# Optimization experiments

Hardware: AMD Instinct MI355X
Metric: run time of the kernel (lower is better)

Reference implementation:

```python
import jax, jax.numpy as jnp
import numpy as np
import math

NUM_HEADS = 16
NUM_KV_HEADS = 4
HEAD_DIM = 128
ROPE_THETA = 10000.0


def rotate_half(x):
    half = x.shape[-1] // 2
    return jnp.concatenate((-x[..., half:], x[..., :half]), axis=-1)


def setup_inputs() -> dict:
    key = jax.random.key(0)
    ks = jax.random.split(key, 5)
    B, S, H = 2, 2048, 2048
    hidden_states = jax.random.normal(ks[0], (B, S, H), dtype=jnp.float32)
    scale = 1.0 / math.sqrt(H)
    wq = jax.random.normal(ks[1], (NUM_HEADS * HEAD_DIM, H), dtype=jnp.float32) * scale
    wk = jax.random.normal(ks[2], (NUM_KV_HEADS * HEAD_DIM, H), dtype=jnp.float32) * scale
    wv = jax.random.normal(ks[3], (NUM_KV_HEADS * HEAD_DIM, H), dtype=jnp.float32) * scale
    wo = jax.random.normal(ks[4], (H, NUM_HEADS * HEAD_DIM), dtype=jnp.float32) * scale
    # additive causal mask [B,1,S,S]
    causal = jnp.where(jnp.tril(jnp.ones((S, S), dtype=bool)), 0.0, -1e9).astype(jnp.float32)
    attention_mask = jnp.broadcast_to(causal[None, None], (B, 1, S, S))
    position_ids = jnp.broadcast_to(jnp.arange(S, dtype=jnp.int64)[None], (B, S))
    return {
        'hidden_states': hidden_states, 'wq': wq, 'wk': wk, 'wv': wv, 'wo': wo,
        'attention_mask': attention_mask, 'position_ids': position_ids,
    }


def reference(hidden_states, wq, wk, wv, wo, attention_mask, position_ids):
    B, S, H = hidden_states.shape
    nh, nkv, hd = NUM_HEADS, NUM_KV_HEADS, HEAD_DIM
    groups = nh // nkv

    # projections (torch Linear: x @ W^T)
    q = (hidden_states @ wq.T).reshape(B, S, nh, hd).transpose(0, 2, 1, 3)   # [B,nh,S,hd]
    k = (hidden_states @ wk.T).reshape(B, S, nkv, hd).transpose(0, 2, 1, 3)  # [B,nkv,S,hd]
    v = (hidden_states @ wv.T).reshape(B, S, nkv, hd).transpose(0, 2, 1, 3)

    # RoPE: cos/sin gathered by position_ids -> [B,1,S,hd]
    inv_freq = 1.0 / (ROPE_THETA ** (jnp.arange(0, hd, 2, dtype=jnp.float32) / hd))  # [hd/2]
    freqs = position_ids.astype(jnp.float32)[:, :, None] * inv_freq                  # [B,S,hd/2]
    emb = jnp.concatenate((freqs, freqs), axis=-1)                                   # [B,S,hd]
    cos = jnp.cos(emb)[:, None]
    sin = jnp.sin(emb)[:, None]
    q = q * cos + rotate_half(q) * sin
    k = k * cos + rotate_half(k) * sin

    # GQA: repeat kv heads
    k = jnp.repeat(k, groups, axis=1)  # [B,nh,S,hd]
    v = jnp.repeat(v, groups, axis=1)

    scores = jnp.einsum('bhqd,bhkd->bhqk', q, k) / math.sqrt(hd) + attention_mask
    attn = jax.nn.softmax(scores.astype(jnp.float32), axis=-1).astype(q.dtype)
    ctx = jnp.einsum('bhqk,bhkd->bhqd', attn, v)            # [B,nh,S,hd]
    ctx = ctx.transpose(0, 2, 1, 3).reshape(B, S, nh * hd)  # [B,S,H]
    out = ctx @ wo.T
    return out
```

## Files before the change

### kernel.cpp

```cpp
#include <hip/hip_runtime.h>
#include <hip/hip_bf16.h>
#include <stdint.h>

typedef __bf16 bf16x8 __attribute__((ext_vector_type(8)));
typedef float f32x4 __attribute__((ext_vector_type(4)));
typedef float f32x16 __attribute__((ext_vector_type(16)));

#define NH 16
#define NKV 4
#define HD 128
#define HQ (NH*HD)
#define HKV (NKV*HD)
#define LDX 3072

__device__ __forceinline__ void gl_lds16(const void* g, void* l) {
  __builtin_amdgcn_global_load_lds(
      (const __attribute__((address_space(1))) void*)g,
      (__attribute__((address_space(3))) void*)l, 16, 0, 0);
}

__device__ __forceinline__ uint32_t pk2(float lo, float hi) {
  union { __hip_bfloat16 h[2]; uint32_t u; } x;
  x.h[0] = __float2bfloat16(lo);
  x.h[1] = __float2bfloat16(hi);
  return x.u;
}

__global__ void k_cast_all(const float* __restrict__ hs, const float* __restrict__ wq,
                           const float* __restrict__ wk, const float* __restrict__ wv,
                           const float* __restrict__ wo,
                           __hip_bfloat16* __restrict__ Xb, __hip_bfloat16* __restrict__ Wqb,
                           __hip_bfloat16* __restrict__ Wkb, __hip_bfloat16* __restrict__ Wvb,
                           __hip_bfloat16* __restrict__ Wob) {
  int i = blockIdx.x * blockDim.x + threadIdx.x;
  const float* src; __hip_bfloat16* dst; int off;
  if (i < 2097152)      { src = hs; dst = Xb;  off = i; }
  else if (i < 3145728) { src = wq; dst = Wqb; off = i - 2097152; }
  else if (i < 3407872) { src = wk; dst = Wkb; off = i - 3145728; }
  else if (i < 3670016) { src = wv; dst = Wvb; off = i - 3407872; }
  else                  { src = wo; dst = Wob; off = i - 3670016; }
  float4 v = reinterpret_cast<const float4*>(src)[off];
  union { __hip_bfloat16 b[4]; ushort4 u; } o;
  o.b[0] = __float2bfloat16(v.x); o.b[1] = __float2bfloat16(v.y);
  o.b[2] = __float2bfloat16(v.z); o.b[3] = __float2bfloat16(v.w);
  reinterpret_cast<ushort4*>(dst)[off] = o.u;
}

__global__ void k_rope_vt(__hip_bfloat16* __restrict__ X, __hip_bfloat16* __restrict__ Vt,
                          const int* __restrict__ pid, int S) {
  __shared__ __hip_bfloat16 tile[32][33];
  const int RB = 4096;
  if (blockIdx.x < RB) {
    int idx = blockIdx.x * 256 + threadIdx.x;
    int i = idx & 63;
    int hh = (idx >> 6) & 3;
    int tok = idx >> 8;
    bool is64 = (pid[1] == 0);
    int pos = is64 ? pid[2 * tok] : pid[tok];
    float f = (float)pos * __expf(-(float)i * (9.210340371976184f / 64.0f));
    float sn, cs;
    __sincosf(f, &sn, &cs);
    size_t base = (size_t)tok * LDX + 2048 + hh * 128;
    float x0 = __bfloat162float(X[base + i]);
    float x1 = __bfloat162float(X[base + 64 + i]);
    X[base + i]      = __float2bfloat16(x0 * cs - x1 * sn);
    X[base + 64 + i] = __float2bfloat16(x1 * cs + x0 * sn);
  } else {
    int bb = blockIdx.x - RB;
    int bkv = bb >> 8;
    int rem = bb & 255;
    int s0 = (rem & 63) * 32, d0 = (rem >> 6) * 32;
    int b = bkv >> 2, kvh = bkv & 3;
    int tx = threadIdx.x & 31, ty = threadIdx.x >> 5;
    for (int i = 0; i < 32; i += 8)
      tile[ty + i][tx] = X[((size_t)(b * S) + s0 + ty + i) * LDX + 2560 + kvh * 128 + d0 + tx];
    __syncthreads();
    for (int i = 0; i < 32; i += 8)
      Vt[((size_t)bkv * 128 + d0 + ty + i) * S + s0 + tx] = tile[tx][ty + i];
  }
}

__global__ __launch_bounds__(512, 1) void k_gemmQKV(
    const __hip_bfloat16* __restrict__ A, const __hip_bfloat16* __restrict__ B,
    __hip_bfloat16* __restrict__ C, int Nld, int K) {
  __shared__ __hip_bfloat16 As[2][2][256 * 32];
  __shared__ __hip_bfloat16 Bs[2][2][192 * 32];

  const int t = threadIdx.x, w = t >> 6, l = t & 63;
  const int lr = l & 15, lg = l >> 4;
  const int wr = w >> 2, wc = w & 3;

  const int bid = blockIdx.x;
  const int id2 = (bid & 7) * 32 + (bid >> 3);
  const int bm = id2 & 15, bn = id2 >> 4;

  const __hip_bfloat16* Ap = A + (size_t)(bm * 256) * K;
  const __hip_bfloat16* Bp = B + (size_t)(bn * 192) * K;

  auto stageA = [&](__hip_bfloat16* lp, int kt, int kk) {
#pragma unroll
    for (int inst = 0; inst < 2; ++inst) {
      const int chunk = inst * 512 + t;
      const int row = chunk >> 2, c_st = chunk & 3;
      const int c_nat = c_st ^ ((row >> 1) & 3);
      gl_lds16(Ap + (size_t)row * K + kt * 64 + kk * 32 + c_nat * 8,
               lp + (size_t)(inst * 512 + (w << 6)) * 8);
    }
  };
  auto stageB = [&](__hip_bfloat16* lp, int kt, int kk) {
    {
      const int chunk = t;
      const int row = chunk >> 2, c_st = chunk & 3;
      const int c_nat = c_st ^ ((row >> 1) & 3);
      gl_lds16(Bp + (size_t)row * K + kt * 64 + kk * 32 + c_nat * 8,
               lp + (size_t)(w << 6) * 8);
    }
    if (w < 4) {
      const int chunk = 512 + t;
      const int row = chunk >> 2, c_st = chunk & 3;
      const int c_nat = c_st ^ ((row >> 1) & 3);
      gl_lds16(Bp + (size_t)row * K + kt * 64 + kk * 32 + c_nat * 8,
               lp + (size_t)(512 + (w << 6)) * 8);
    }
  };
  auto waitTile = [&](int wv) {
    if (wv < 4) asm volatile("s_waitcnt vmcnt(4)" ::: "memory");
    else        asm volatile("s_waitcnt vmcnt(3)" ::: "memory");
  };

  f32x4 acc[8][3] = {};
  const int nt = K >> 6;

  stageA(As[0][0], 0, 0);
  stageB(Bs[0][0], 0, 0);
  stageA(As[0][1], 0, 1);
  stageB(Bs[0][1], 0, 1);
  stageA(As[1][0], 1, 0);
  stageB(Bs[1][0], 1, 0);
  waitTile(w);
  __builtin_amdgcn_s_barrier();
  asm volatile("" ::: "memory");

  for (int tt = 0; tt < nt; ++tt) {
    const int cur = tt & 1;
    const int nx1 = (tt + 1 < nt) ? tt + 1 : nt - 1;
    const int nx2 = (tt + 2 < nt) ? tt + 2 : nt - 1;
#pragma unroll
    for (int kk = 0; kk < 2; ++kk) {
      bf16x8 aF[8], bF[3];
#pragma unroll
      for (int n = 0; n < 3; ++n) {
        int rB = wc * 48 + n * 16 + lr;
        bF[n] = *reinterpret_cast<const bf16x8*>(
            &Bs[cur][kk][rB * 32 + (lg ^ ((rB >> 1) & 3)) * 8]);
      }
#pragma unroll
      for (int m8 = 0; m8 < 8; ++m8) {
        int rA = wr * 128 + (m8 >> 2) * 64 + (m8 & 3) * 16 + lr;
        aF[m8] = *reinterpret_cast<const bf16x8*>(
            &As[cur][kk][rA * 32 + (lg ^ ((rA >> 1) & 3)) * 8]);
      }
      if (kk == 0) { stageA(As[nx1 & 1][1], nx1, 1); stageB(Bs[nx1 & 1][1], nx1, 1); }
      else         { stageA(As[nx2 & 1][0], nx2, 0); stageB(Bs[nx2 & 1][0], nx2, 0); }
      asm volatile("" ::: "memory");
      __builtin_amdgcn_s_barrier();
      asm volatile("" ::: "memory");
      __builtin_amdgcn_s_setprio(1);
#pragma unroll
      for (int m8 = 0; m8 < 8; ++m8)
#pragma unroll
        for (int n = 0; n < 3; ++n)
          acc[m8][n] = __builtin_amdgcn_mfma_f32_16x16x32_bf16(
              aF[m8], bF[n], acc[m8][n], 0, 0, 0);
      __builtin_amdgcn_s_setprio(0);
      if (kk == 1) waitTile(w);
      asm volatile("" ::: "memory");
      __builtin_amdgcn_s_barrier();
      asm volatile("" ::: "memory");
    }
  }

  const int row0 = bm * 256 + wr * 128;
  const int col0 = bn * 192 + wc * 48;
#pragma unroll
  for (int m = 0; m < 8; ++m)
#pragma unroll
    for (int n = 0; n < 3; ++n)
#pragma unroll
      for (int r = 0; r < 4; ++r)
        C[(size_t)(row0 + (m >> 2) * 64 + (m & 3) * 16 + lg * 4 + r) * Nld +
          col0 + n * 16 + lr] = __float2bfloat16(acc[m][n][r]);
}

__global__ __launch_bounds__(512, 1) void k_gemmO(
    const __hip_bfloat16* __restrict__ A, const __hip_bfloat16* __restrict__ B,
    float* __restrict__ C, int N, int K) {
  __shared__ __hip_bfloat16 As[2][2][128 * 32];
  __shared__ __hip_bfloat16 Bs[2][2][256 * 32];

  const int t = threadIdx.x, w = t >> 6, l = t & 63;
  const int lr = l & 15, lg = l >> 4;
  const int wr = w >> 2, wc = w & 3;

  const int bid = blockIdx.x;
  const int id2 = (bid & 7) * 32 + (bid >> 3);
  const int bm = id2 & 31, bn = id2 >> 5;

  const __hip_bfloat16* Ap = A + (size_t)(bm * 128) * K;
  const __hip_bfloat16* Bp = B + (size_t)(bn * 256) * K;

  auto stageA = [&](__hip_bfloat16* lp, int kt, int kk) {
    const int row = t >> 2, c_st = t & 3;
    const int c_nat = c_st ^ ((row >> 1) & 3);
    gl_lds16(Ap + (size_t)row * K + kt * 64 + kk * 32 + c_nat * 8,
             lp + (size_t)(w << 6) * 8);
  };
  auto stageB = [&](__hip_bfloat16* lp, int kt, int kk) {
#pragma unroll
    for (int inst = 0; inst < 2; ++inst) {
      const int chunk = inst * 512 + t;
      const int row = chunk >> 2, c_st = chunk & 3;
      const int c_nat = c_st ^ ((row >> 1) & 3);
      gl_lds16(Bp + (size_t)row * K + kt * 64 + kk * 32 + c_nat * 8,
               lp + (size_t)(inst * 512 + (w << 6)) * 8);
    }
  };

  f32x4 acc[4][4] = {};
  const int nt = K >> 6;

  stageA(As[0][0], 0, 0);
  stageB(Bs[0][0], 0, 0);
  stageA(As[0][1], 0, 1);
  stageB(Bs[0][1], 0, 1);
  stageA(As[1][0], 1, 0);
  stageB(Bs[1][0], 1, 0);
  asm volatile("s_waitcnt vmcnt(3)" ::: "memory");
  __builtin_amdgcn_s_barrier();
  asm volatile("" ::: "memory");

  for (int tt = 0; tt < nt; ++tt) {
    const int cur = tt & 1;
    const int nx1 = (tt + 1 < nt) ? tt + 1 : nt - 1;
    const int nx2 = (tt + 2 < nt) ? tt + 2 : nt - 1;
#pragma unroll
    for (int kk = 0; kk < 2; ++kk) {
      bf16x8 aF[4], bF[4];
#pragma unroll
      for (int n = 0; n < 4; ++n) {
        int rB = wc * 64 + n * 16 + lr;
        bF[n] = *reinterpret_cast<const bf16x8*>(
            &Bs[cur][kk][rB * 32 + (lg ^ ((rB >> 1) & 3)) * 8]);
      }
#pragma unroll
      for (int m4 = 0; m4 < 4; ++m4) {
        int rA = wr * 64 + (m4 >> 1) * 32 + (m4 & 1) * 16 + lr;
        aF[m4] = *reinterpret_cast<const bf16x8*>(
            &As[cur][kk][rA * 32 + (lg ^ ((rA >> 1) & 3)) * 8]);
      }
      if (kk == 0) { stageA(As[nx1 & 1][1], nx1, 1); stageB(Bs[nx1 & 1][1], nx1, 1); }
      else         { stageA(As[nx2 & 1][0], nx2, 0); stageB(Bs[nx2 & 1][0], nx2, 0); }
      asm volatile("" ::: "memory");
      __builtin_amdgcn_s_barrier();
      asm volatile("" ::: "memory");
      __builtin_amdgcn_s_setprio(1);
#pragma unroll
      for (int m4 = 0; m4 < 4; ++m4)
#pragma unroll
        for (int n = 0; n < 4; ++n)
          acc[m4][n] = __builtin_amdgcn_mfma_f32_16x16x32_bf16(
              aF[m4], bF[n], acc[m4][n], 0, 0, 0);
      __builtin_amdgcn_s_setprio(0);
      if (kk == 1) asm volatile("s_waitcnt vmcnt(3)" ::: "memory");
      asm volatile("" ::: "memory");
      __builtin_amdgcn_s_barrier();
      asm volatile("" ::: "memory");
    }
  }

  const int row0 = bm * 128 + wr * 64;
  const int col0 = bn * 256 + wc * 64;
#pragma unroll
  for (int m = 0; m < 4; ++m)
#pragma unroll
    for (int n = 0; n < 4; ++n)
#pragma unroll
      for (int r = 0; r < 4; ++r)
        C[(size_t)(row0 + m * 16 + lg * 4 + r) * N + col0 + n * 16 + lr] =
            acc[m][n][r];
}

__global__ __launch_bounds__(256, 2) void k_attn(
    const __hip_bfloat16* __restrict__ X, const __hip_bfloat16* __restrict__ Vt,
    const int* __restrict__ pid, __hip_bfloat16* __restrict__ ctx, int S) {
  __shared__ __hip_bfloat16 SM[32768];

  const int bid = blockIdx.x;
  const int g  = bid & 7;
  const int idx = bid >> 3;
  int hi, jj;
  if (idx < 32) { hi = idx >> 4;              jj = idx & 15; }
  else          { hi = 2 + ((idx - 32) >> 4); jj = 15 - ((idx - 32) & 15); }
  const int b = g >> 2, kvh = g & 3;
  const int h = kvh * 4 + hi;

  const int t = threadIdx.x, w = t >> 6, l = t & 63;
  const int q = l & 31, hf = l >> 5;
  const int qt64 = (w < 2) ? jj : (31 - jj);
  const int q0w = qt64 * 64 + (w & 1) * 32;
  const int nt = 32 - jj;
  const float c1 = 0.12752511f;
  const float M0 = 48.0f;

  const __hip_bfloat16* Qp = X + ((size_t)(b * S) + q0w + q) * LDX + h * 128 + hf * 8;
  bf16x8 aq[8];
#pragma unroll
  for (int mq = 0; mq < 8; ++mq)
    aq[mq] = *reinterpret_cast<const bf16x8*>(Qp + mq * 16);

  {
    bool is64 = (pid[1] == 0);
    int toki = b * S + q0w + q;
    int pos = is64 ? pid[2 * toki] : pid[toki];
    float fpos = (float)pos;
#pragma unroll
    for (int mq = 0; mq < 4; ++mq)
#pragma unroll
      for (int j = 0; j < 8; ++j) {
        int fi = mq * 16 + hf * 8 + j;
        float ang = fpos * __expf((float)fi * (-9.210340371976184f / 64.0f));
        float sn, cs;
        __sincosf(ang, &sn, &cs);
        float x0 = (float)aq[mq][j];
        float x1 = (float)aq[mq + 4][j];
        aq[mq][j]     = (__bf16)(x0 * cs - x1 * sn);
        aq[mq + 4][j] = (__bf16)(x1 * cs + x0 * sn);
      }
  }

  const __hip_bfloat16* KG = X + (size_t)(b * S) * LDX + 2048 + kvh * 128;
  const __hip_bfloat16* VG = Vt + ((size_t)(b * NKV + kvh) * 128) * S;

  auto stageK = [&](int buf, int kv0) {
#pragma unroll
    for (int j = 0; j < 4; ++j) {
      int off16 = (w * 4 + j) * 64 + l;
      int row = off16 >> 4;
      int c_nat = (off16 & 15) ^ ((row >> 1) & 15);
      gl_lds16(KG + (size_t)(kv0 + row) * LDX + c_nat * 8,
               &SM[buf * 8192 + (w * 4 + j) * 512]);
    }
  };
  auto stageV = [&](int buf, int kv0) {
#pragma unroll
    for (int j = 0; j < 4; ++j) {
      int off16 = (w * 4 + j) * 64 + l;
      int d = off16 >> 3;
      int c_nat = (off16 & 7) ^ ((d >> 2) & 7);
      gl_lds16(VG + (size_t)d * S + kv0 + c_nat * 8,
               &SM[16384 + buf * 8192 + (w * 4 + j) * 512]);
    }
  };

  f32x16 O[4] = {};
  float l_i = 0.0f;

  stageK(0, 0); stageV(0, 0);
  int cur = 0;
  for (int tkv = 0; tkv < nt; ++tkv) {
    const int kv0 = tkv * 64;
    if (tkv + 1 < nt) {
      stageK(cur ^ 1, kv0 + 64);
      stageV(cur ^ 1, kv0 + 64);
      asm volatile("s_waitcnt vmcnt(8)" ::: "memory");
    } else {
      asm volatile("s_waitcnt vmcnt(0)" ::: "memory");
    }
    __builtin_amdgcn_sched_barrier(0);
    __builtin_amdgcn_s_barrier();
    asm volatile("" ::: "memory");

    if (kv0 <= q0w + 31) {
      const __hip_bfloat16* Ksb = &SM[cur * 8192];
      const __hip_bfloat16* Vsb = &SM[16384 + cur * 8192];

      f32x16 p[2];
      __builtin_amdgcn_s_setprio(1);
#pragma unroll
      for (int sb = 0; sb < 2; ++sb) {
        f32x16 s0 = {}, s1 = {};
#pragma unroll
        for (int mm = 0; mm < 4; ++mm) {
          int arow = sb * 32 + q;
          int swz = (arow >> 1) & 15;
          int c0 = (4 * mm + hf) ^ swz;
          int c1i = (4 * mm + 2 + hf) ^ swz;
          bf16x8 kf0 = *reinterpret_cast<const bf16x8*>(&Ksb[arow * 128 + c0 * 8]);
          bf16x8 kf1 = *reinterpret_cast<const bf16x8*>(&Ksb[arow * 128 + c1i * 8]);
          s0 = __builtin_amdgcn_mfma_f32_32x32x16_bf16(kf0, aq[2 * mm], s0, 0, 0, 0);
          s1 = __builtin_amdgcn_mfma_f32_32x32x16_bf16(kf1, aq[2 * mm + 1], s1, 0, 0, 0);
        }
        p[sb] = s0 + s1;
      }
      __builtin_amdgcn_s_setprio(0);

      if (kv0 + 63 > q0w) {
#pragma unroll
        for (int sb = 0; sb < 2; ++sb)
#pragma unroll
          for (int r = 0; r < 16; ++r) {
            int kv_abs = kv0 + sb * 32 + (r & 3) + 8 * (r >> 2) + 4 * hf;
            if (kv_abs > q0w + q) p[sb][r] = -3.0e38f;
          }
      }

      float rs = 0.0f;
#pragma unroll
      for (int sb = 0; sb < 2; ++sb)
#pragma unroll
        for (int r = 0; r < 16; ++r) {
          float e = exp2f((p[sb][r] - M0) * c1);
          p[sb][r] = e;
          rs += e;
        }
      rs += __shfl_xor(rs, 32, 64);
      l_i += rs;

      uint32_t pku[2][8];
#pragma unroll
      for (int sb = 0; sb < 2; ++sb)
#pragma unroll
        for (int gp = 0; gp < 4; ++gp) {
          pku[sb][gp * 2 + 0] = pk2(p[sb][gp * 4 + 0], p[sb][gp * 4 + 1]);
          pku[sb][gp * 2 + 1] = pk2(p[sb][gp * 4 + 2], p[sb][gp * 4 + 3]);
        }

      __builtin_amdgcn_s_setprio(1);
#pragma unroll
      for (int kk = 0; kk < 4; ++kk) {
        const int sb = kk >> 1, bs = (kk & 1) * 4;
        union { uint32_t u[4]; bf16x8 v; } pf;
        uint32_t x0 = pku[sb][bs + 0], x2 = pku[sb][bs + 2];
        uint32_t x1 = pku[sb][bs + 1], x3 = pku[sb][bs + 3];
        asm("v_permlane32_swap_b32 %0, %1" : "+v"(x0), "+v"(x2));
        asm("v_permlane32_swap_b32 %0, %1" : "+v"(x1), "+v"(x3));
        pf.u[0] = x0; pf.u[1] = x1; pf.u[2] = x2; pf.u[3] = x3;
#pragma unroll
        for (int db = 0; db < 4; ++db) {
          int vrow = db * 32 + q;
          int c_lds = (2 * kk + hf) ^ ((vrow >> 2) & 7);
          bf16x8 vf = *reinterpret_cast<const bf16x8*>(&Vsb[vrow * 64 + c_lds * 8]);
          O[db] = __builtin_amdgcn_mfma_f32_32x32x16_bf16(vf, pf.v, O[db], 0, 0, 0);
        }
      }
      __builtin_amdgcn_s_setprio(0);
    }
    asm volatile("" ::: "memory");
    __builtin_amdgcn_s_barrier();
    asm volatile("" ::: "memory");
    cur ^= 1;
  }

  float inv = 1.0f / l_i;
  __hip_bfloat16* Lo = &SM[w * 4352];
#pragma unroll
  for (int db = 0; db < 4; ++db)
#pragma unroll
    for (int rr = 0; rr < 4; ++rr) {
      int d0 = db * 32 + rr * 8 + hf * 4;
      uint32_t u0 = pk2(O[db][rr * 4 + 0] * inv, O[db][rr * 4 + 1] * inv);
      uint32_t u1 = pk2(O[db][rr * 4 + 2] * inv, O[db][rr * 4 + 3] * inv);
      *reinterpret_cast<uint2*>(&Lo[q * 136 + d0]) = make_uint2(u0, u1);
    }
  __syncthreads();
#pragma unroll
  for (int it = 0; it < 8; ++it) {
    int row = it * 4 + (l >> 4), c = l & 15;
    bf16x8 vv = *reinterpret_cast<const bf16x8*>(&Lo[row * 136 + c * 8]);
    *reinterpret_cast<bf16x8*>(
        &ctx[((size_t)(b * S) + q0w + row) * HQ + h * 128 + c * 8]) = vv;
  }
}

extern "C" void kernel_launch(void* const* d_in, const int* in_sizes, int n_in,
                              void* d_out, int out_size, void* d_ws, size_t ws_size,
                              hipStream_t stream) {
  const int B = 2, S = 2048, H = 2048;
  const int M = B * S;

  const float* hs = (const float*)d_in[0];
  const float* wq = (const float*)d_in[1];
  const float* wk = (const float*)d_in[2];
  const float* wv = (const float*)d_in[3];
  const float* wo = (const float*)d_in[4];
  const int* pid = (const int*)d_in[6];

  char* p = (char*)d_ws;
  auto carve = [&](size_t bytes) {
    void* r = (void*)p;
    p += (bytes + 255) & ~(size_t)255;
    return r;
  };
  __hip_bfloat16* Xb   = (__hip_bfloat16*)carve((size_t)M * H * 2);
  __hip_bfloat16* Wqb  = (__hip_bfloat16*)carve((size_t)HQ * H * 2);
  __hip_bfloat16* Wkb  = (__hip_bfloat16*)carve((size_t)HKV * H * 2);
  __hip_bfloat16* Wvb  = (__hip_bfloat16*)carve((size_t)HKV * H * 2);
  __hip_bfloat16* Wob  = (__hip_bfloat16*)carve((size_t)H * HQ * 2);
  __hip_bfloat16* XQKV = (__hip_bfloat16*)carve((size_t)M * LDX * 2);
  __hip_bfloat16* Vtb  = (__hip_bfloat16*)carve((size_t)M * HKV * 2);
  __hip_bfloat16* Ctx  = (__hip_bfloat16*)carve((size_t)M * HQ * 2);

  k_cast_all<<<18432, 256, 0, stream>>>(hs, wq, wk, wv, wo, Xb, Wqb, Wkb, Wvb, Wob);

  k_gemmQKV<<<dim3(256), 512, 0, stream>>>(Xb, Wqb, XQKV, LDX, H);

  k_rope_vt<<<dim3(4096 + 2048), 256, 0, stream>>>(XQKV, Vtb, pid, S);

  k_attn<<<dim3(512), 256, 0, stream>>>(XQKV, Vtb, pid, Ctx, S);

  k_gemmO<<<dim3(256), 512, 0, stream>>>(Ctx, Wob, (float*)d_out, H, HQ);
}
```

Measured before the change: 206.2 us.

## Make attention persistent with atomic work queue and split KV across warp pairs

The attention kernel becomes persistent: blocks pull work items (64-query tiles per head) from a global atomic counter, longest tiles first, instead of using a fixed paired-tile mapping. Within a block, the four waves now split each 64-key tile into two 32-key halves per 32-query slab, and the two partial O/l results are combined through shared memory at the end. This aims to improve load balance and per-wave work granularity. The cost is an atomic per item, extra LDS reduction and syncs, and half the MFMA work per wave per iteration. The counter is reset in the preceding rope kernel.

```diff
diff --git a/kernel.cpp b/kernel.cpp
--- a/kernel.cpp
+++ b/kernel.cpp
@@ -47,8 +47,9 @@
 }
 
 __global__ void k_rope_vt(__hip_bfloat16* __restrict__ X, __hip_bfloat16* __restrict__ Vt,
-                          const int* __restrict__ pid, int S) {
+                          const int* __restrict__ pid, int* __restrict__ ctr, int S) {
   __shared__ __hip_bfloat16 tile[32][33];
+  if (blockIdx.x == 0 && threadIdx.x == 0) *ctr = 0;
   const int RB = 4096;
   if (blockIdx.x < RB) {
     int idx = blockIdx.x * 256 + threadIdx.x;
@@ -292,193 +293,222 @@
 
 __global__ __launch_bounds__(256, 2) void k_attn(
     const __hip_bfloat16* __restrict__ X, const __hip_bfloat16* __restrict__ Vt,
-    const int* __restrict__ pid, __hip_bfloat16* __restrict__ ctx, int S) {
+    const int* __restrict__ pid, __hip_bfloat16* __restrict__ ctx,
+    int* __restrict__ ctr, int S) {
   __shared__ __hip_bfloat16 SM[32768];
-
-  const int bid = blockIdx.x;
-  const int g  = bid & 7;
-  const int idx = bid >> 3;
-  int hi, jj;
-  if (idx < 32) { hi = idx >> 4;              jj = idx & 15; }
-  else          { hi = 2 + ((idx - 32) >> 4); jj = 15 - ((idx - 32) & 15); }
-  const int b = g >> 2, kvh = g & 3;
-  const int h = kvh * 4 + hi;
+  __shared__ int sh_item;
 
   const int t = threadIdx.x, w = t >> 6, l = t & 63;
   const int q = l & 31, hf = l >> 5;
-  const int qt64 = (w < 2) ? jj : (31 - jj);
-  const int q0w = qt64 * 64 + (w & 1) * 32;
-  const int nt = 32 - jj;
+  const int kvhalf = w >> 1;
   const float c1 = 0.12752511f;
   const float M0 = 48.0f;
-
-  const __hip_bfloat16* Qp = X + ((size_t)(b * S) + q0w + q) * LDX + h * 128 + hf * 8;
-  bf16x8 aq[8];
-#pragma unroll
-  for (int mq = 0; mq < 8; ++mq)
-    aq[mq] = *reinterpret_cast<const bf16x8*>(Qp + mq * 16);
-
-  {
-    bool is64 = (pid[1] == 0);
-    int toki = b * S + q0w + q;
-    int pos = is64 ? pid[2 * toki] : pid[toki];
-    float fpos = (float)pos;
-#pragma unroll
-    for (int mq = 0; mq < 4; ++mq)
-#pragma unroll
-      for (int j = 0; j < 8; ++j) {
-        int fi = mq * 16 + hf * 8 + j;
-        float ang = fpos * __expf((float)fi * (-9.210340371976184f / 64.0f));
-        float sn, cs;
-        __sincosf(ang, &sn, &cs);
-        float x0 = (float)aq[mq][j];
-        float x1 = (float)aq[mq + 4][j];
-        aq[mq][j]     = (__bf16)(x0 * cs - x1 * sn);
-        aq[mq + 4][j] = (__bf16)(x1 * cs + x0 * sn);
-      }
-  }
-
-  const __hip_bfloat16* KG = X + (size_t)(b * S) * LDX + 2048 + kvh * 128;
-  const __hip_bfloat16* VG = Vt + ((size_t)(b * NKV + kvh) * 128) * S;
-
-  auto stageK = [&](int buf, int kv0) {
-#pragma unroll
-    for (int j = 0; j < 4; ++j) {
-      int off16 = (w * 4 + j) * 64 + l;
-      int row = off16 >> 4;
-      int c_nat = (off16 & 15) ^ ((row >> 1) & 15);
-      gl_lds16(KG + (size_t)(kv0 + row) * LDX + c_nat * 8,
-               &SM[buf * 8192 + (w * 4 + j) * 512]);
-    }
-  };
-  auto stageV = [&](int buf, int kv0) {
-#pragma unroll
-    for (int j = 0; j < 4; ++j) {
-      int off16 = (w * 4 + j) * 64 + l;
-      int d = off16 >> 3;
-      int c_nat = (off16 & 7) ^ ((d >> 2) & 7);
-      gl_lds16(VG + (size_t)d * S + kv0 + c_nat * 8,
-               &SM[16384 + buf * 8192 + (w * 4 + j) * 512]);
-    }
-  };
-
-  f32x16 O[4] = {};
-  float l_i = 0.0f;
-
-  stageK(0, 0); stageV(0, 0);
-  int cur = 0;
-  for (int tkv = 0; tkv < nt; ++tkv) {
-    const int kv0 = tkv * 64;
-    if (tkv + 1 < nt) {
-      stageK(cur ^ 1, kv0 + 64);
-      stageV(cur ^ 1, kv0 + 64);
-      asm volatile("s_waitcnt vmcnt(8)" ::: "memory");
-    } else {
-      asm volatile("s_waitcnt vmcnt(0)" ::: "memory");
-    }
-    __builtin_amdgcn_sched_barrier(0);
-    __builtin_amdgcn_s_barrier();
-    asm volatile("" ::: "memory");
-
-    if (kv0 <= q0w + 31) {
-      const __hip_bfloat16* Ksb = &SM[cur * 8192];
-      const __hip_bfloat16* Vsb = &SM[16384 + cur * 8192];
-
-      f32x16 p[2];
-      __builtin_amdgcn_s_setprio(1);
-#pragma unroll
-      for (int sb = 0; sb < 2; ++sb) {
-        f32x16 s0 = {}, s1 = {};
-#pragma unroll
-        for (int mm = 0; mm < 4; ++mm) {
-          int arow = sb * 32 + q;
-          int swz = (arow >> 1) & 15;
-          int c0 = (4 * mm + hf) ^ swz;
-          int c1i = (4 * mm + 2 + hf) ^ swz;
-          bf16x8 kf0 = *reinterpret_cast<const bf16x8*>(&Ksb[arow * 128 + c0 * 8]);
-          bf16x8 kf1 = *reinterpret_cast<const bf16x8*>(&Ksb[arow * 128 + c1i * 8]);
-          s0 = __builtin_amdgcn_mfma_f32_32x32x16_bf16(kf0, aq[2 * mm], s0, 0, 0, 0);
-          s1 = __builtin_amdgcn_mfma_f32_32x32x16_bf16(kf1, aq[2 * mm + 1], s1, 0, 0, 0);
-        }
-        p[sb] = s0 + s1;
-      }
-      __builtin_amdgcn_s_setprio(0);
-
-      if (kv0 + 63 > q0w) {
-#pragma unroll
-        for (int sb = 0; sb < 2; ++sb)
+  const bool is64 = (pid[1] == 0);
+
+  for (;;) {
+    if (t == 0) sh_item = atomicAdd(ctr, 1);
+    __syncthreads();
+    const int item = sh_item;
+    if (item >= 1024) return;
+    const int j  = 31 - (item >> 5);
+    const int gh = item & 31;
+    const int g = gh & 7, hi = gh >> 3;
+    const int b = g >> 2, kvh = g & 3;
+    const int h = kvh * 4 + hi;
+    const int q0w = (2 * j + (w & 1)) * 32;
+    const int nt = j + 1;
+
+    const __hip_bfloat16* Qp = X + ((size_t)(b * S) + q0w + q) * LDX + h * 128 + hf * 8;
+    bf16x8 aq[8];
+#pragma unroll
+    for (int mq = 0; mq < 8; ++mq)
+      aq[mq] = *reinterpret_cast<const bf16x8*>(Qp + mq * 16);
+    {
+      int toki = b * S + q0w + q;
+      int pos = is64 ? pid[2 * toki] : pid[toki];
+      float fpos = (float)pos;
+#pragma unroll
+      for (int mq = 0; mq < 4; ++mq)
+#pragma unroll
+        for (int jj = 0; jj < 8; ++jj) {
+          int fi = mq * 16 + hf * 8 + jj;
+          float ang = fpos * __expf((float)fi * (-9.210340371976184f / 64.0f));
+          float sn, cs;
+          __sincosf(ang, &sn, &cs);
+          float x0 = (float)aq[mq][jj];
+          float x1 = (float)aq[mq + 4][jj];
+          aq[mq][jj]     = (__bf16)(x0 * cs - x1 * sn);
+          aq[mq + 4][jj] = (__bf16)(x1 * cs + x0 * sn);
+        }
+    }
+
+    const __hip_bfloat16* KG = X + (size_t)(b * S) * LDX + 2048 + kvh * 128;
+    const __hip_bfloat16* VG = Vt + ((size_t)(b * NKV + kvh) * 128) * S;
+
+    auto stageK = [&](int buf, int kv0) {
+#pragma unroll
+      for (int jj = 0; jj < 4; ++jj) {
+        int off16 = (w * 4 + jj) * 64 + l;
+        int row = off16 >> 4;
+        int c_nat = (off16 & 15) ^ ((row >> 1) & 15);
+        gl_lds16(KG + (size_t)(kv0 + row) * LDX + c_nat * 8,
+                 &SM[buf * 8192 + (w * 4 + jj) * 512]);
+      }
+    };
+    auto stageV = [&](int buf, int kv0) {
+#pragma unroll
+      for (int jj = 0; jj < 4; ++jj) {
+        int off16 = (w * 4 + jj) * 64 + l;
+        int d = off16 >> 3;
+        int c_nat = (off16 & 7) ^ ((d >> 2) & 7);
+        gl_lds16(VG + (size_t)d * S + kv0 + c_nat * 8,
+                 &SM[16384 + buf * 8192 + (w * 4 + jj) * 512]);
+      }
+    };
+
+    f32x16 O[4] = {};
+    float l_i = 0.0f;
+
+    stageK(0, 0); stageV(0, 0);
+    int cur = 0;
+    for (int tkv = 0; tkv < nt; ++tkv) {
+      const int kvbase = tkv * 64 + kvhalf * 32;
+      if (tkv + 1 < nt) {
+        stageK(cur ^ 1, tkv * 64 + 64);
+        stageV(cur ^ 1, tkv * 64 + 64);
+        asm volatile("s_waitcnt vmcnt(8)" ::: "memory");
+      } else {
+        asm volatile("s_waitcnt vmcnt(0)" ::: "memory");
+      }
+      __builtin_amdgcn_sched_barrier(0);
+      __builtin_amdgcn_s_barrier();
+      asm volatile("" ::: "memory");
+
+      if (kvbase <= q0w + 31) {
+        const __hip_bfloat16* Ksb = &SM[cur * 8192];
+        const __hip_bfloat16* Vsb = &SM[16384 + cur * 8192];
+
+        f32x16 p;
+        {
+          f32x16 s0 = {}, s1 = {};
+          const int arow = kvhalf * 32 + q;
+          const int swz = (arow >> 1) & 15;
+          __builtin_amdgcn_s_setprio(1);
+#pragma unroll
+          for (int mm = 0; mm < 4; ++mm) {
+            int c0 = (4 * mm + hf) ^ swz;
+            int c1i = (4 * mm + 2 + hf) ^ swz;
+            bf16x8 kf0 = *reinterpret_cast<const bf16x8*>(&Ksb[arow * 128 + c0 * 8]);
+            bf16x8 kf1 = *reinterpret_cast<const bf16x8*>(&Ksb[arow * 128 + c1i * 8]);
+            s0 = __builtin_amdgcn_mfma_f32_32x32x16_bf16(kf0, aq[2 * mm], s0, 0, 0, 0);
+            s1 = __builtin_amdgcn_mfma_f32_32x32x16_bf16(kf1, aq[2 * mm + 1], s1, 0, 0, 0);
+          }
+          __builtin_amdgcn_s_setprio(0);
+          p = s0 + s1;
+        }
+
+        if (kvbase + 31 > q0w) {
 #pragma unroll
           for (int r = 0; r < 16; ++r) {
-            int kv_abs = kv0 + sb * 32 + (r & 3) + 8 * (r >> 2) + 4 * hf;
-            if (kv_abs > q0w + q) p[sb][r] = -3.0e38f;
+            int kv_abs = kvbase + (r & 3) + 8 * (r >> 2) + 4 * hf;
+            if (kv_abs > q0w + q) p[r] = -3.0e38f;
           }
-      }
-
-      float rs = 0.0f;
-#pragma unroll
-      for (int sb = 0; sb < 2; ++sb)
+        }
+
+        float rs = 0.0f;
 #pragma unroll
         for (int r = 0; r < 16; ++r) {
-          float e = exp2f((p[sb][r] - M0) * c1);
-          p[sb][r] = e;
+          float e = exp2f((p[r] - M0) * c1);
+          p[r] = e;
           rs += e;
         }
-      rs += __shfl_xor(rs, 32, 64);
-      l_i += rs;
-
-      uint32_t pku[2][8];
-#pragma unroll
-      for (int sb = 0; sb < 2; ++sb)
+        rs += __shfl_xor(rs, 32, 64);
+        l_i += rs;
+
+        uint32_t pku[8];
 #pragma unroll
         for (int gp = 0; gp < 4; ++gp) {
-          pku[sb][gp * 2 + 0] = pk2(p[sb][gp * 4 + 0], p[sb][gp * 4 + 1]);
-          pku[sb][gp * 2 + 1] = pk2(p[sb][gp * 4 + 2], p[sb][gp * 4 + 3]);
-        }
-
-      __builtin_amdgcn_s_setprio(1);
-#pragma unroll
-      for (int kk = 0; kk < 4; ++kk) {
-        const int sb = kk >> 1, bs = (kk & 1) * 4;
-        union { uint32_t u[4]; bf16x8 v; } pf;
-        uint32_t x0 = pku[sb][bs + 0], x2 = pku[sb][bs + 2];
-        uint32_t x1 = pku[sb][bs + 1], x3 = pku[sb][bs + 3];
-        asm("v_permlane32_swap_b32 %0, %1" : "+v"(x0), "+v"(x2));
-        asm("v_permlane32_swap_b32 %0, %1" : "+v"(x1), "+v"(x3));
-        pf.u[0] = x0; pf.u[1] = x1; pf.u[2] = x2; pf.u[3] = x3;
-#pragma unroll
-        for (int db = 0; db < 4; ++db) {
-          int vrow = db * 32 + q;
-          int c_lds = (2 * kk + hf) ^ ((vrow >> 2) & 7);
-          bf16x8 vf = *reinterpret_cast<const bf16x8*>(&Vsb[vrow * 64 + c_lds * 8]);
-          O[db] = __builtin_amdgcn_mfma_f32_32x32x16_bf16(vf, pf.v, O[db], 0, 0, 0);
-        }
-      }
-      __builtin_amdgcn_s_setprio(0);
-    }
-    asm volatile("" ::: "memory");
-    __builtin_amdgcn_s_barrier();
-    asm volatile("" ::: "memory");
-    cur ^= 1;
-  }
-
-  float inv = 1.0f / l_i;
-  __hip_bfloat16* Lo = &SM[w * 4352];
-#pragma unroll
-  for (int db = 0; db < 4; ++db)
-#pragma unroll
-    for (int rr = 0; rr < 4; ++rr) {
-      int d0 = db * 32 + rr * 8 + hf * 4;
-      uint32_t u0 = pk2(O[db][rr * 4 + 0] * inv, O[db][rr * 4 + 1] * inv);
-      uint32_t u1 = pk2(O[db][rr * 4 + 2] * inv, O[db][rr * 4 + 3] * inv);
-      *reinterpret_cast<uint2*>(&Lo[q * 136 + d0]) = make_uint2(u0, u1);
-    }
-  __syncthreads();
-#pragma unroll
-  for (int it = 0; it < 8; ++it) {
-    int row = it * 4 + (l >> 4), c = l & 15;
-    bf16x8 vv = *reinterpret_cast<const bf16x8*>(&Lo[row * 136 + c * 8]);
-    *reinterpret_cast<bf16x8*>(
-        &ctx[((size_t)(b * S) + q0w + row) * HQ + h * 128 + c * 8]) = vv;
+          pku[gp * 2 + 0] = pk2(p[gp * 4 + 0], p[gp * 4 + 1]);
+          pku[gp * 2 + 1] = pk2(p[gp * 4 + 2], p[gp * 4 + 3]);
+        }
+
+        __builtin_amdgcn_s_setprio(1);
+#pragma unroll
+        for (int kk = 0; kk < 2; ++kk) {
+          union { uint32_t u[4]; bf16x8 v; } pf;
+          uint32_t x0 = pku[4 * kk + 0], x2 = pku[4 * kk + 2];
+          uint32_t x1 = pku[4 * kk + 1], x3 = pku[4 * kk + 3];
+          asm("v_permlane32_swap_b32 %0, %1" : "+v"(x0), "+v"(x2));
+          asm("v_permlane32_swap_b32 %0, %1" : "+v"(x1), "+v"(x3));
+          pf.u[0] = x0; pf.u[1] = x1; pf.u[2] = x2; pf.u[3] = x3;
+#pragma unroll
+          for (int db = 0; db < 4; ++db) {
+            int vrow = db * 32 + q;
+            int cc = (4 * kvhalf + 2 * kk + hf) ^ ((vrow >> 2) & 7);
+            bf16x8 vf = *reinterpret_cast<const bf16x8*>(&Vsb[vrow * 64 + cc * 8]);
+            O[db] = __builtin_amdgcn_mfma_f32_32x32x16_bf16(vf, pf.v, O[db], 0, 0, 0);
+          }
+        }
+        __builtin_amdgcn_s_setprio(0);
+      }
+      asm volatile("" ::: "memory");
+      __builtin_amdgcn_s_barrier();
+      asm volatile("" ::: "memory");
+      cur ^= 1;
+    }
+
+    float* fSM = reinterpret_cast<float*>(SM);
+    if (w >= 2) {
+      float* dst = fSM + (w - 2) * 4096 + l * 64;
+#pragma unroll
+      for (int db = 0; db < 4; ++db)
+#pragma unroll
+        for (int rr = 0; rr < 4; ++rr) {
+          f32x4 v4 = { O[db][rr * 4 + 0], O[db][rr * 4 + 1],
+                       O[db][rr * 4 + 2], O[db][rr * 4 + 3] };
+          *reinterpret_cast<f32x4*>(dst + db * 16 + rr * 4) = v4;
+        }
+      fSM[8192 + (w - 2) * 64 + l] = l_i;
+    }
+    __syncthreads();
+    if (w < 2) {
+      const float* src = fSM + w * 4096 + l * 64;
+#pragma unroll
+      for (int db = 0; db < 4; ++db)
+#pragma unroll
+        for (int rr = 0; rr < 4; ++rr) {
+          f32x4 v4 = *reinterpret_cast<const f32x4*>(src + db * 16 + rr * 4);
+          O[db][rr * 4 + 0] += v4[0]; O[db][rr * 4 + 1] += v4[1];
+          O[db][rr * 4 + 2] += v4[2]; O[db][rr * 4 + 3] += v4[3];
+        }
+      l_i += fSM[8192 + w * 64 + l];
+    }
+    __syncthreads();
+
+    if (w < 2) {
+      float inv = 1.0f / l_i;
+      __hip_bfloat16* Lo = &SM[w * 4352];
+#pragma unroll
+      for (int db = 0; db < 4; ++db)
+#pragma unroll
+        for (int rr = 0; rr < 4; ++rr) {
+          int d0 = db * 32 + rr * 8 + hf * 4;
+          uint32_t u0 = pk2(O[db][rr * 4 + 0] * inv, O[db][rr * 4 + 1] * inv);
+          uint32_t u1 = pk2(O[db][rr * 4 + 2] * inv, O[db][rr * 4 + 3] * inv);
+          *reinterpret_cast<uint2*>(&Lo[q * 136 + d0]) = make_uint2(u0, u1);
+        }
+    }
+    __syncthreads();
+    if (w < 2) {
+      __hip_bfloat16* Lo = &SM[w * 4352];
+#pragma unroll
+      for (int it = 0; it < 8; ++it) {
+        int row = it * 4 + (l >> 4), c = l & 15;
+        bf16x8 vv = *reinterpret_cast<const bf16x8*>(&Lo[row * 136 + c * 8]);
+        *reinterpret_cast<bf16x8*>(
+            &ctx[((size_t)(b * S) + q0w + row) * HQ + h * 128 + c * 8]) = vv;
+      }
+    }
   }
 }
 
@@ -509,14 +539,15 @@
   __hip_bfloat16* XQKV = (__hip_bfloat16*)carve((size_t)M * LDX * 2);
   __hip_bfloat16* Vtb  = (__hip_bfloat16*)carve((size_t)M * HKV * 2);
   __hip_bfloat16* Ctx  = (__hip_bfloat16*)carve((size_t)M * HQ * 2);
+  int* ctr = (int*)carve(256);
 
   k_cast_all<<<18432, 256, 0, stream>>>(hs, wq, wk, wv, wo, Xb, Wqb, Wkb, Wvb, Wob);
 
   k_gemmQKV<<<dim3(256), 512, 0, stream>>>(Xb, Wqb, XQKV, LDX, H);
 
-  k_rope_vt<<<dim3(4096 + 2048), 256, 0, stream>>>(XQKV, Vtb, pid, S);
-
-  k_attn<<<dim3(512), 256, 0, stream>>>(XQKV, Vtb, pid, Ctx, S);
+  k_rope_vt<<<dim3(4096 + 2048), 256, 0, stream>>>(XQKV, Vtb, pid, ctr, S);
+
+  k_attn<<<dim3(512), 256, 0, stream>>>(XQKV, Vtb, pid, Ctx, ctr, S);
 
   k_gemmO<<<dim3(256), 512, 0, stream>>>(Ctx, Wob, (float*)d_out, H, HQ);
 }
```

After: 208.9 us. Within noise of the previous version (+1.3%).
